# Performance work log

Hardware: AMD Instinct MI355X
Metric: run time of the kernel (lower is better)

Reference implementation:

```python
import jax, jax.numpy as jnp
import numpy as np

B_SZ = 512
D1_IN = 40    # input_dim_first (features)
T = 1024      # input_dim_second (time)
D1_OUT = 120  # output_dim_first
D2_OUT = 64   # output_dim_second


def setup_inputs() -> dict:
    key = jax.random.key(0)
    k_x, k_w1, k_w2, k_b = jax.random.split(key, 4)
    x = jax.random.normal(k_x, (B_SZ, D1_IN, T), dtype=jnp.float32)
    # kaiming-uniform-like init for W1/W2, faithful W init: zeros with 1/T diagonal
    bound1 = 1.0 / np.sqrt(D1_IN)
    W1 = jax.random.uniform(k_w1, (D1_OUT, D1_IN), minval=-bound1, maxval=bound1, dtype=jnp.float32)
    W = jnp.eye(T, dtype=jnp.float32) / T
    bound2 = 1.0 / np.sqrt(T)
    W2 = jax.random.uniform(k_w2, (T, D2_OUT), minval=-bound2, maxval=bound2, dtype=jnp.float32)
    B = jax.random.uniform(k_b, (D1_OUT, D2_OUT), minval=-bound1, maxval=bound1, dtype=jnp.float32)
    lambda_param = jnp.full((1,), 0.5, dtype=jnp.float32)
    return {"x": x, "W1": W1, "W": W, "W2": W2, "B": B, "lambda_param": lambda_param}


def reference(x, W1, W, W2, B, lambda_param):
    # X_bar[b] = W1 @ x[b]  -> [B, D1_OUT, T]
    X_bar = jnp.einsum("of,bft->bot", W1, x)
    # E[b] = x[b] @ W       -> [B, D1_IN, T]; softmax over time axis
    E = jnp.einsum("bft,ts->bfs", x, W)
    A = jax.nn.softmax(E, axis=2)
    lam = jnp.clip(lambda_param, 0.0, 1.0)  # scalar in [1]
    # gather attention rows via modulo indexing: row j uses A[:, j % D1_IN]
    idx = jnp.arange(D1_OUT) % D1_IN
    A_g = A[:, idx, :]                       # [B, D1_OUT, T]
    X_tilde = lam * X_bar * A_g + (1.0 - lam) * X_bar
    out = jnp.einsum("bot,ts->bos", X_tilde, W2) + B[None, :, :]
    out = jax.nn.relu(out)
    return (out, A)
```

## Files before the change

### kernel.cpp

```cpp
#include <hip/hip_runtime.h>
#include <cstdint>
#include <cstddef>

typedef __attribute__((ext_vector_type(8))) short bf16x8;
typedef __attribute__((ext_vector_type(4))) float f32x4;
typedef __attribute__((ext_vector_type(4))) unsigned short ushort4v;
typedef __attribute__((ext_vector_type(2))) unsigned int uint2v;

#define B_SZ   512
#define D1_IN  40
#define T_DIM  1024
#define D1_OUT 120
#define D2_OUT 64
#define OUT0_SZ (B_SZ * D1_OUT * D2_OUT)

__device__ unsigned int g_wmask[8];

__device__ __forceinline__ unsigned short f2bf(float f) {
    unsigned int u = __float_as_uint(f);
    u += 0x7FFFu + ((u >> 16) & 1u);
    return (unsigned short)(u >> 16);
}
__device__ __forceinline__ float bf2f(unsigned int h) {
    return __uint_as_float(h << 16);
}
__device__ __forceinline__ void gld16v(const void* g, void* l) {
    __builtin_amdgcn_global_load_lds(
        (const __attribute__((address_space(1))) unsigned int*)g,
        (__attribute__((address_space(3))) unsigned int*)l, 16, 0, 0);
}

__global__ __launch_bounds__(256) void k_prep_small(const float* __restrict__ W1,
                                                    const float* __restrict__ W,
                                                    const float* __restrict__ W2,
                                                    unsigned short* __restrict__ w2g,
                                                    unsigned short* __restrict__ w1p) {
    int blk = blockIdx.x, tid = threadIdx.x;
    if (blk < 64) {
        __shared__ float tile[32][33];
        int c0 = (blk & 1) * 32, r0 = (blk >> 1) * 32;
        int tx = tid & 31, ty = tid >> 5;
        #pragma unroll
        for (int i = 0; i < 4; i++)
            tile[ty + i * 8][tx] = W2[(size_t)(r0 + ty + i * 8) * D2_OUT + c0 + tx];
        __syncthreads();
        #pragma unroll
        for (int i = 0; i < 4; i++) {
            int s = c0 + ty + i * 8;
            int t = r0 + tx;
            size_t idx = ((size_t)(t >> 6) * 64 + s) * 64
                       + ((((t >> 3) & 7) ^ (s & 7)) << 3) + (t & 7);
            w2g[idx] = f2bf(tile[tx][ty + i * 8]);
        }
    } else if (blk < 72) {
        __shared__ unsigned int sm[256];
        int bn = blk - 64;
        int rbase = tid >> 5, c0 = (tid & 31) * 4;
        unsigned int m = 0;
        for (int ks = 0; ks < 32; ks++) {
            bool nz = false;
            #pragma unroll
            for (int i = 0; i < 4; i++) {
                int r = ks * 32 + rbase + i * 8;
                float4 v = *(const float4*)(W + (size_t)r * T_DIM + bn * 128 + c0);
                nz |= (v.x != 0.f) | (v.y != 0.f) | (v.z != 0.f) | (v.w != 0.f);
            }
            if (nz) m |= (1u << ks);
        }
        sm[tid] = m;
        __syncthreads();
        if (tid == 0) {
            unsigned int acc = 0;
            for (int i = 0; i < 256; i++) acc |= sm[i];
            g_wmask[bn] = acc;
        }
    } else {
        for (int i = tid; i < 128 * 64; i += 256) {
            int o = i >> 6, f = i & 63;
            w1p[i] = (o < D1_OUT && f < D1_IN) ? f2bf(W1[o * D1_IN + f]) : (unsigned short)0;
        }
    }
}

__global__ __launch_bounds__(256) void k_wfrag(const float* __restrict__ W,
                                               unsigned short* __restrict__ wfrag) {
    __shared__ float tl[32 * 132];
    int bn = blockIdx.x >> 5, ks = blockIdx.x & 31;
    int tid = threadIdx.x;
    int k0 = ks * 32, c0 = bn * 128;
    for (int i = tid; i < 1024; i += 256) {
        int r = i >> 5, c4 = i & 31;
        float4 v = *(const float4*)(W + (size_t)(k0 + r) * T_DIM + c0 + c4 * 4);
        *(float4*)&tl[r * 132 + c4 * 4] = v;
    }
    __syncthreads();
    int l = tid & 63, v = tid >> 6;
    int rr = l & 15, q = l >> 4;
    #pragma unroll
    for (int nn = 0; nn < 2; nn++) {
        int n = v + nn * 4;
        bf16x8 o;
        #pragma unroll
        for (int j = 0; j < 8; j++)
            o[j] = (short)f2bf(tl[(q * 8 + j) * 132 + n * 16 + rr]);
        *(bf16x8*)(wfrag + (((size_t)(bn * 32 + ks) * 8 + n) * 512) + (size_t)l * 8) = o;
    }
}

__global__ __launch_bounds__(512) void k_gemm1sm(const float* __restrict__ x,
                                                 const unsigned short* __restrict__ wfrag,
                                                 const float* __restrict__ lamp,
                                                 float* __restrict__ A,
                                                 unsigned short* __restrict__ gab) {
    __shared__ unsigned short xs[16 * 1032];
    __shared__ float red[16][9];
    int row0 = blockIdx.x * 16;
    int tid = threadIdx.x, l = tid & 63, w = tid >> 6;
    int rr = l & 15, q = l >> 4;
    unsigned int mask = g_wmask[w];
    float lam = fminf(fmaxf(lamp[0], 0.f), 1.f), oml = 1.f - lam;
    f32x4 acc[8] = {};

    {
        int r = tid >> 5, c = tid & 31;
        const float* xrow = x + (size_t)(row0 + r) * T_DIM;
        #pragma unroll
        for (int it = 0; it < 8; it++) {
            int c4 = c + it * 32;
            float4 v = *(const float4*)(xrow + c4 * 4);
            ushort4v o;
            o.x = (unsigned short)(__float_as_uint(v.x) >> 16);
            o.y = (unsigned short)(__float_as_uint(v.y) >> 16);
            o.z = (unsigned short)(__float_as_uint(v.z) >> 16);
            o.w = (unsigned short)(__float_as_uint(v.w) >> 16);
            *(ushort4v*)&xs[r * 1032 + c4 * 4] = o;
        }
    }
    __syncthreads();

    for (int ks = 0; ks < 32; ks++) {
        if (!((mask >> ks) & 1u)) continue;
        bf16x8 bx = *(const bf16x8*)&xs[rr * 1032 + ks * 32 + q * 8];
        const unsigned short* wp = wfrag + ((size_t)(w * 32 + ks) * 8) * 512 + (size_t)l * 8;
        #pragma unroll
        for (int n = 0; n < 8; n++) {
            bf16x8 af = *(const bf16x8*)(wp + (size_t)n * 512);
            acc[n] = __builtin_amdgcn_mfma_f32_16x16x32_bf16(af, bx, acc[n], 0, 0, 0);
        }
    }

    float mx = -3.4e38f;
    #pragma unroll
    for (int n = 0; n < 8; n++)
        #pragma unroll
        for (int jj = 0; jj < 4; jj++) mx = fmaxf(mx, acc[n][jj]);
    mx = fmaxf(mx, __shfl_xor(mx, 16));
    mx = fmaxf(mx, __shfl_xor(mx, 32));
    if (l < 16) red[rr][w] = mx;
    __syncthreads();
    float g = red[rr][0];
    #pragma unroll
    for (int ww = 1; ww < 8; ww++) g = fmaxf(g, red[rr][ww]);
    __syncthreads();
    float s = 0.f;
    #pragma unroll
    for (int n = 0; n < 8; n++)
        #pragma unroll
        for (int jj = 0; jj < 4; jj++) {
            float p = __expf(acc[n][jj] - g);
            acc[n][jj] = p;
            s += p;
        }
    s += __shfl_xor(s, 16);
    s += __shfl_xor(s, 32);
    if (l < 16) red[rr][w] = s;
    __syncthreads();
    float tot = 0.f;
    #pragma unroll
    for (int ww = 0; ww < 8; ww++) tot += red[rr][ww];
    float inv = 1.f / tot;
    int rowA = row0 + rr;
    size_t rowg = (size_t)rowA * T_DIM + w * 128;
    int bb = rowA / D1_IN, ff = rowA % D1_IN;
    size_t gbase = (size_t)bb * 16 * 2560 + (size_t)ff * 64;
    #pragma unroll
    for (int n = 0; n < 8; n++) {
        f32x4 o;
        o.x = acc[n][0] * inv; o.y = acc[n][1] * inv;
        o.z = acc[n][2] * inv; o.w = acc[n][3] * inv;
        *(f32x4*)&A[rowg + n * 16 + q * 4] = o;
        int t = w * 128 + n * 16 + q * 4;
        uint2v pk;
        pk.x = (unsigned int)f2bf(lam * o.x + oml) | ((unsigned int)f2bf(lam * o.y + oml) << 16);
        pk.y = (unsigned int)f2bf(lam * o.z + oml) | ((unsigned int)f2bf(lam * o.w + oml) << 16);
        *(uint2v*)&gab[gbase + (size_t)(t >> 6) * 2560 + (t & 63)] = pk;
    }
}

__global__ __launch_bounds__(512) void k_fused(const float* __restrict__ x,
                                               const unsigned short* __restrict__ gab,
                                               const unsigned short* __restrict__ w1p,
                                               const unsigned short* __restrict__ w2g,
                                               const float* __restrict__ Bias,
                                               float* __restrict__ out) {
    __shared__ float xfst[2][10 * 260];
    __shared__ unsigned short gs16[2][5 * 528];
    __shared__ unsigned short w2s[64 * 64];
    __shared__ unsigned short xbt[64 * 72];
    __shared__ unsigned short xtl[128 * 72];
    int b = blockIdx.x;
    int tid = threadIdx.x, l = tid & 63, w = tid >> 6;
    int rr = l & 15, q = l >> 4;
    bf16x8 aw[2];
    #pragma unroll
    for (int ks = 0; ks < 2; ks++)
        aw[ks] = *(const bf16x8*)(w1p + (w * 16 + rr) * 64 + ks * 32 + q * 8);
    int og = w * 16 + rr;
    int am = og % D1_IN;
    int gofs = (am >> 3) * 528 + (am & 7) * 64;
    f32x4 acc2[4] = {};
    const float* xb = x + (size_t)b * D1_IN * T_DIM;
    const unsigned short* gb = gab + (size_t)b * 16 * 2560;

    auto STAGE_XG = [&](int buf, int tc) {
        int t0 = tc * 64;
        int f = w * 4 + (l >> 4);
        gld16v(xb + (size_t)f * T_DIM + t0 + (l & 15) * 4, &xfst[buf][w * 260]);
        if (w < 2) {
            int f2 = 32 + w * 4 + (l >> 4);
            gld16v(xb + (size_t)f2 * T_DIM + t0 + (l & 15) * 4, &xfst[buf][(8 + w) * 260]);
        }
        if (w < 5)
            gld16v(gb + (size_t)tc * 2560 + w * 512 + l * 8, &gs16[buf][w * 528]);
    };
    auto STAGE_W2 = [&](int tc) {
        gld16v(w2g + (size_t)tc * 4096 + w * 512 + l * 8, &w2s[w * 512]);
    };
    auto CONVERT = [&](int buf) {
        if (tid < 320) {
            int g = tid >> 5, tp = tid & 31;
            const float* src = &xfst[buf][g * 260 + 2 * tp];
            float a0 = src[0],   b0 = src[1];
            float a1 = src[64],  b1 = src[65];
            float a2 = src[128], b2 = src[129];
            float a3 = src[192], b3 = src[193];
            uint2v lo, hi;
            lo.x = (unsigned int)f2bf(a0) | ((unsigned int)f2bf(a1) << 16);
            lo.y = (unsigned int)f2bf(a2) | ((unsigned int)f2bf(a3) << 16);
            hi.x = (unsigned int)f2bf(b0) | ((unsigned int)f2bf(b1) << 16);
            hi.y = (unsigned int)f2bf(b2) | ((unsigned int)f2bf(b3) << 16);
            int t = 2 * tp;
            *(uint2v*)&xbt[t * 72 + g * 4] = lo;
            *(uint2v*)&xbt[(t + 1) * 72 + g * 4] = hi;
        }
    };

    {
        int t = tid >> 3, k = tid & 7;
        *(uint2v*)&xbt[t * 72 + 40 + k * 4] = (uint2v){0u, 0u};
    }
    STAGE_XG(0, 0);
    __syncthreads();
    for (int tc = 0; tc < 16; tc++) {
        int cur = tc & 1;
        CONVERT(cur);
        STAGE_W2(tc);
        __syncthreads();
        if (tc < 15) STAGE_XG(cur ^ 1, tc + 1);
        f32x4 acc1[4] = {};
        #pragma unroll
        for (int ni = 0; ni < 4; ni++)
            #pragma unroll
            for (int ks = 0; ks < 2; ks++) {
                bf16x8 bx = *(const bf16x8*)&xbt[(ni * 16 + rr) * 72 + ks * 32 + q * 8];
                acc1[ni] = __builtin_amdgcn_mfma_f32_16x16x32_bf16(bx, aw[ks], acc1[ni], 0, 0, 0);
            }
        const unsigned short* gr = &gs16[cur][gofs];
        #pragma unroll
        for (int ni = 0; ni < 4; ni++) {
            uint2 gp = *(const uint2*)(gr + ni * 16 + q * 4);
            float e0 = acc1[ni][0] * bf2f(gp.x & 0xFFFFu);
            float e1 = acc1[ni][1] * bf2f(gp.x >> 16);
            float e2 = acc1[ni][2] * bf2f(gp.y & 0xFFFFu);
            float e3 = acc1[ni][3] * bf2f(gp.y >> 16);
            uint2 pk;
            pk.x = (unsigned int)f2bf(e0) | ((unsigned int)f2bf(e1) << 16);
            pk.y = (unsigned int)f2bf(e2) | ((unsigned int)f2bf(e3) << 16);
            *(uint2*)&xtl[og * 72 + ni * 16 + q * 4] = pk;
        }
        #pragma unroll
        for (int ks2 = 0; ks2 < 2; ks2++) {
            bf16x8 a2 = *(const bf16x8*)&xtl[og * 72 + ks2 * 32 + q * 8];
            #pragma unroll
            for (int ni = 0; ni < 4; ni++) {
                int s = ni * 16 + rr;
                bf16x8 b2 = *(const bf16x8*)&w2s[s * 64 + (((ks2 * 4 + q) ^ (s & 7)) << 3)];
                acc2[ni] = __builtin_amdgcn_mfma_f32_16x16x32_bf16(a2, b2, acc2[ni], 0, 0, 0);
            }
        }
        __syncthreads();
    }
    #pragma unroll
    for (int ni = 0; ni < 4; ni++)
        #pragma unroll
        for (int j = 0; j < 4; j++) {
            int row = w * 16 + q * 4 + j;
            if (row < D1_OUT) {
                int col = ni * 16 + rr;
                float v = acc2[ni][j] + Bias[row * D2_OUT + col];
                out[((size_t)b * D1_OUT + row) * D2_OUT + col] = fmaxf(v, 0.f);
            }
        }
}

extern "C" void kernel_launch(void* const* d_in, const int* in_sizes, int n_in,
                              void* d_out, int out_size, void* d_ws, size_t ws_size,
                              hipStream_t stream) {
    const float* x    = (const float*)d_in[0];
    const float* W1   = (const float*)d_in[1];
    const float* W    = (const float*)d_in[2];
    const float* W2   = (const float*)d_in[3];
    const float* Bias = (const float*)d_in[4];
    const float* lam  = (const float*)d_in[5];
    float* out = (float*)d_out;
    float* A   = out + OUT0_SZ;

    char* ws = (char*)d_ws;
    unsigned short* gab   = (unsigned short*)(ws);
    unsigned short* wfrag = (unsigned short*)(ws + 41943040);
    unsigned short* w2g   = (unsigned short*)(ws + 44040192);
    unsigned short* w1p   = (unsigned short*)(ws + 44171264);

    hipLaunchKernelGGL(k_prep_small, dim3(73), dim3(256), 0, stream, W1, W, W2, w2g, w1p);
    hipLaunchKernelGGL(k_wfrag, dim3(256), dim3(256), 0, stream, W, wfrag);
    hipLaunchKernelGGL(k_gemm1sm, dim3(1280), dim3(512), 0, stream, x, wfrag, lam, A, gab);
    hipLaunchKernelGGL(k_fused, dim3(512), dim3(512), 0, stream, x, gab, w1p, w2g, Bias, out);
}
```

Baseline: 114.8 us.

## Drop bf16 gate buffer; read fp32 A in fused kernel, persistent softmax kernel

The softmax kernel no longer writes a separate bf16 gating tensor (lam*A+1-lam). The fused kernel now streams the fp32 A output directly and applies the lambda blend in registers. This removes a 40MB-class intermediate write and its layout transform, at the cost of reading A in fp32, twice the bytes of the old gate read. The softmax kernel also becomes persistent with 512 blocks and double-buffers the x tile, prefetching the next rows into registers while it computes.

```diff
diff --git a/kernel.cpp b/kernel.cpp
--- a/kernel.cpp
+++ b/kernel.cpp
@@ -20,9 +20,6 @@
     unsigned int u = __float_as_uint(f);
     u += 0x7FFFu + ((u >> 16) & 1u);
     return (unsigned short)(u >> 16);
-}
-__device__ __forceinline__ float bf2f(unsigned int h) {
-    return __uint_as_float(h << 16);
 }
 __device__ __forceinline__ void gld16v(const void* g, void* l) {
     __builtin_amdgcn_global_load_lds(
@@ -109,129 +106,129 @@
 
 __global__ __launch_bounds__(512) void k_gemm1sm(const float* __restrict__ x,
                                                  const unsigned short* __restrict__ wfrag,
-                                                 const float* __restrict__ lamp,
-                                                 float* __restrict__ A,
-                                                 unsigned short* __restrict__ gab) {
-    __shared__ unsigned short xs[16 * 1032];
-    __shared__ float red[16][9];
-    int row0 = blockIdx.x * 16;
+                                                 float* __restrict__ A) {
+    __shared__ unsigned short xs[2][16 * 1032];
+    __shared__ float red[2][16][9];
     int tid = threadIdx.x, l = tid & 63, w = tid >> 6;
     int rr = l & 15, q = l >> 4;
+    int r = tid >> 5, c = tid & 31;
     unsigned int mask = g_wmask[w];
-    float lam = fminf(fmaxf(lamp[0], 0.f), 1.f), oml = 1.f - lam;
-    f32x4 acc[8] = {};
-
+
+    f32x4 xv[8];
     {
-        int r = tid >> 5, c = tid & 31;
-        const float* xrow = x + (size_t)(row0 + r) * T_DIM;
+        const float* xrow = x + (size_t)(blockIdx.x * 16 + r) * T_DIM;
+        #pragma unroll
+        for (int it = 0; it < 8; it++)
+            xv[it] = *(const f32x4*)(xrow + (c + it * 32) * 4);
+    }
+    int buf = 0;
+    for (int p = blockIdx.x; p < 1280; p += 512, buf ^= 1) {
         #pragma unroll
         for (int it = 0; it < 8; it++) {
-            int c4 = c + it * 32;
-            float4 v = *(const float4*)(xrow + c4 * 4);
             ushort4v o;
-            o.x = (unsigned short)(__float_as_uint(v.x) >> 16);
-            o.y = (unsigned short)(__float_as_uint(v.y) >> 16);
-            o.z = (unsigned short)(__float_as_uint(v.z) >> 16);
-            o.w = (unsigned short)(__float_as_uint(v.w) >> 16);
-            *(ushort4v*)&xs[r * 1032 + c4 * 4] = o;
-        }
-    }
-    __syncthreads();
-
-    for (int ks = 0; ks < 32; ks++) {
-        if (!((mask >> ks) & 1u)) continue;
-        bf16x8 bx = *(const bf16x8*)&xs[rr * 1032 + ks * 32 + q * 8];
-        const unsigned short* wp = wfrag + ((size_t)(w * 32 + ks) * 8) * 512 + (size_t)l * 8;
+            o.x = (unsigned short)(__float_as_uint(xv[it].x) >> 16);
+            o.y = (unsigned short)(__float_as_uint(xv[it].y) >> 16);
+            o.z = (unsigned short)(__float_as_uint(xv[it].z) >> 16);
+            o.w = (unsigned short)(__float_as_uint(xv[it].w) >> 16);
+            *(ushort4v*)&xs[buf][r * 1032 + (c + it * 32) * 4] = o;
+        }
+        __syncthreads();
+        int pn = p + 512;
+        if (pn < 1280) {
+            const float* xrow = x + (size_t)(pn * 16 + r) * T_DIM;
+            #pragma unroll
+            for (int it = 0; it < 8; it++)
+                xv[it] = *(const f32x4*)(xrow + (c + it * 32) * 4);
+        }
+        f32x4 acc[8] = {};
+        for (int ks = 0; ks < 32; ks++) {
+            if (!((mask >> ks) & 1u)) continue;
+            bf16x8 bx = *(const bf16x8*)&xs[buf][rr * 1032 + ks * 32 + q * 8];
+            const unsigned short* wp = wfrag + ((size_t)(w * 32 + ks) * 8) * 512 + (size_t)l * 8;
+            #pragma unroll
+            for (int n = 0; n < 8; n++) {
+                bf16x8 af = *(const bf16x8*)(wp + (size_t)n * 512);
+                acc[n] = __builtin_amdgcn_mfma_f32_16x16x32_bf16(af, bx, acc[n], 0, 0, 0);
+            }
+        }
+        float mx = -3.4e38f;
+        #pragma unroll
+        for (int n = 0; n < 8; n++)
+            #pragma unroll
+            for (int jj = 0; jj < 4; jj++) mx = fmaxf(mx, acc[n][jj]);
+        mx = fmaxf(mx, __shfl_xor(mx, 16));
+        mx = fmaxf(mx, __shfl_xor(mx, 32));
+        if (l < 16) red[buf][rr][w] = mx;
+        __syncthreads();
+        float g = red[buf][rr][0];
+        #pragma unroll
+        for (int ww = 1; ww < 8; ww++) g = fmaxf(g, red[buf][rr][ww]);
+        __syncthreads();
+        float s = 0.f;
+        #pragma unroll
+        for (int n = 0; n < 8; n++)
+            #pragma unroll
+            for (int jj = 0; jj < 4; jj++) {
+                float pp = __expf(acc[n][jj] - g);
+                acc[n][jj] = pp;
+                s += pp;
+            }
+        s += __shfl_xor(s, 16);
+        s += __shfl_xor(s, 32);
+        if (l < 16) red[buf][rr][w] = s;
+        __syncthreads();
+        float tot = 0.f;
+        #pragma unroll
+        for (int ww = 0; ww < 8; ww++) tot += red[buf][rr][ww];
+        float inv = 1.f / tot;
+        size_t rowg = (size_t)(p * 16 + rr) * T_DIM + w * 128;
         #pragma unroll
         for (int n = 0; n < 8; n++) {
-            bf16x8 af = *(const bf16x8*)(wp + (size_t)n * 512);
-            acc[n] = __builtin_amdgcn_mfma_f32_16x16x32_bf16(af, bx, acc[n], 0, 0, 0);
-        }
-    }
-
-    float mx = -3.4e38f;
-    #pragma unroll
-    for (int n = 0; n < 8; n++)
-        #pragma unroll
-        for (int jj = 0; jj < 4; jj++) mx = fmaxf(mx, acc[n][jj]);
-    mx = fmaxf(mx, __shfl_xor(mx, 16));
-    mx = fmaxf(mx, __shfl_xor(mx, 32));
-    if (l < 16) red[rr][w] = mx;
-    __syncthreads();
-    float g = red[rr][0];
-    #pragma unroll
-    for (int ww = 1; ww < 8; ww++) g = fmaxf(g, red[rr][ww]);
-    __syncthreads();
-    float s = 0.f;
-    #pragma unroll
-    for (int n = 0; n < 8; n++)
-        #pragma unroll
-        for (int jj = 0; jj < 4; jj++) {
-            float p = __expf(acc[n][jj] - g);
-            acc[n][jj] = p;
-            s += p;
-        }
-    s += __shfl_xor(s, 16);
-    s += __shfl_xor(s, 32);
-    if (l < 16) red[rr][w] = s;
-    __syncthreads();
-    float tot = 0.f;
-    #pragma unroll
-    for (int ww = 0; ww < 8; ww++) tot += red[rr][ww];
-    float inv = 1.f / tot;
-    int rowA = row0 + rr;
-    size_t rowg = (size_t)rowA * T_DIM + w * 128;
-    int bb = rowA / D1_IN, ff = rowA % D1_IN;
-    size_t gbase = (size_t)bb * 16 * 2560 + (size_t)ff * 64;
-    #pragma unroll
-    for (int n = 0; n < 8; n++) {
-        f32x4 o;
-        o.x = acc[n][0] * inv; o.y = acc[n][1] * inv;
-        o.z = acc[n][2] * inv; o.w = acc[n][3] * inv;
-        *(f32x4*)&A[rowg + n * 16 + q * 4] = o;
-        int t = w * 128 + n * 16 + q * 4;
-        uint2v pk;
-        pk.x = (unsigned int)f2bf(lam * o.x + oml) | ((unsigned int)f2bf(lam * o.y + oml) << 16);
-        pk.y = (unsigned int)f2bf(lam * o.z + oml) | ((unsigned int)f2bf(lam * o.w + oml) << 16);
-        *(uint2v*)&gab[gbase + (size_t)(t >> 6) * 2560 + (t & 63)] = pk;
+            f32x4 o;
+            o.x = acc[n][0] * inv; o.y = acc[n][1] * inv;
+            o.z = acc[n][2] * inv; o.w = acc[n][3] * inv;
+            *(f32x4*)&A[rowg + n * 16 + q * 4] = o;
+        }
     }
 }
 
 __global__ __launch_bounds__(512) void k_fused(const float* __restrict__ x,
-                                               const unsigned short* __restrict__ gab,
+                                               const float* __restrict__ A,
                                                const unsigned short* __restrict__ w1p,
                                                const unsigned short* __restrict__ w2g,
                                                const float* __restrict__ Bias,
+                                               const float* __restrict__ lamp,
                                                float* __restrict__ out) {
     __shared__ float xfst[2][10 * 260];
-    __shared__ unsigned short gs16[2][5 * 528];
+    __shared__ float gst[2][10 * 260];
     __shared__ unsigned short w2s[64 * 64];
     __shared__ unsigned short xbt[64 * 72];
     __shared__ unsigned short xtl[128 * 72];
     int b = blockIdx.x;
     int tid = threadIdx.x, l = tid & 63, w = tid >> 6;
     int rr = l & 15, q = l >> 4;
+    float lam = fminf(fmaxf(lamp[0], 0.f), 1.f), oml = 1.f - lam;
     bf16x8 aw[2];
     #pragma unroll
     for (int ks = 0; ks < 2; ks++)
         aw[ks] = *(const bf16x8*)(w1p + (w * 16 + rr) * 64 + ks * 32 + q * 8);
     int og = w * 16 + rr;
     int am = og % D1_IN;
-    int gofs = (am >> 3) * 528 + (am & 7) * 64;
+    int amg = (am >> 2) * 260 + (am & 3) * 64;
     f32x4 acc2[4] = {};
     const float* xb = x + (size_t)b * D1_IN * T_DIM;
-    const unsigned short* gb = gab + (size_t)b * 16 * 2560;
+    const float* Ab = A + (size_t)b * D1_IN * T_DIM;
 
     auto STAGE_XG = [&](int buf, int tc) {
         int t0 = tc * 64;
         int f = w * 4 + (l >> 4);
         gld16v(xb + (size_t)f * T_DIM + t0 + (l & 15) * 4, &xfst[buf][w * 260]);
+        gld16v(Ab + (size_t)f * T_DIM + t0 + (l & 15) * 4, &gst[buf][w * 260]);
         if (w < 2) {
             int f2 = 32 + w * 4 + (l >> 4);
             gld16v(xb + (size_t)f2 * T_DIM + t0 + (l & 15) * 4, &xfst[buf][(8 + w) * 260]);
-        }
-        if (w < 5)
-            gld16v(gb + (size_t)tc * 2560 + w * 512 + l * 8, &gs16[buf][w * 528]);
+            gld16v(Ab + (size_t)f2 * T_DIM + t0 + (l & 15) * 4, &gst[buf][(8 + w) * 260]);
+        }
     };
     auto STAGE_W2 = [&](int tc) {
         gld16v(w2g + (size_t)tc * 4096 + w * 512 + l * 8, &w2s[w * 512]);
@@ -275,14 +272,14 @@
                 bf16x8 bx = *(const bf16x8*)&xbt[(ni * 16 + rr) * 72 + ks * 32 + q * 8];
                 acc1[ni] = __builtin_amdgcn_mfma_f32_16x16x32_bf16(bx, aw[ks], acc1[ni], 0, 0, 0);
             }
-        const unsigned short* gr = &gs16[cur][gofs];
+        const float* gr = &gst[cur][amg];
         #pragma unroll
         for (int ni = 0; ni < 4; ni++) {
-            uint2 gp = *(const uint2*)(gr + ni * 16 + q * 4);
-            float e0 = acc1[ni][0] * bf2f(gp.x & 0xFFFFu);
-            float e1 = acc1[ni][1] * bf2f(gp.x >> 16);
-            float e2 = acc1[ni][2] * bf2f(gp.y & 0xFFFFu);
-            float e3 = acc1[ni][3] * bf2f(gp.y >> 16);
+            f32x4 gv = *(const f32x4*)(gr + ni * 16 + q * 4);
+            float e0 = acc1[ni][0] * (lam * gv.x + oml);
+            float e1 = acc1[ni][1] * (lam * gv.y + oml);
+            float e2 = acc1[ni][2] * (lam * gv.z + oml);
+            float e3 = acc1[ni][3] * (lam * gv.w + oml);
             uint2 pk;
             pk.x = (unsigned int)f2bf(e0) | ((unsigned int)f2bf(e1) << 16);
             pk.y = (unsigned int)f2bf(e2) | ((unsigned int)f2bf(e3) << 16);
@@ -326,13 +323,12 @@
     float* A   = out + OUT0_SZ;
 
     char* ws = (char*)d_ws;
-    unsigned short* gab   = (unsigned short*)(ws);
-    unsigned short* wfrag = (unsigned short*)(ws + 41943040);
-    unsigned short* w2g   = (unsigned short*)(ws + 44040192);
-    unsigned short* w1p   = (unsigned short*)(ws + 44171264);
+    unsigned short* wfrag = (unsigned short*)(ws);
+    unsigned short* w2g   = (unsigned short*)(ws + 2097152);
+    unsigned short* w1p   = (unsigned short*)(ws + 2228224);
 
     hipLaunchKernelGGL(k_prep_small, dim3(73), dim3(256), 0, stream, W1, W, W2, w2g, w1p);
     hipLaunchKernelGGL(k_wfrag, dim3(256), dim3(256), 0, stream, W, wfrag);
-    hipLaunchKernelGGL(k_gemm1sm, dim3(1280), dim3(512), 0, stream, x, wfrag, lam, A, gab);
-    hipLaunchKernelGGL(k_fused, dim3(512), dim3(512), 0, stream, x, gab, w1p, w2g, Bias, out);
-}
+    hipLaunchKernelGGL(k_gemm1sm, dim3(512), dim3(512), 0, stream, x, wfrag, A);
+    hipLaunchKernelGGL(k_fused, dim3(512), dim3(512), 0, stream, x, A, w1p, w2g, Bias, lam, out);
+}
```

Measured after the change: 245.9 us. 2.14x slower.

## Fuse softmax attention GEMM into per-batch fused kernel

Applied to the files above, without the earlier changes.

Merges the attention GEMM+softmax kernel into the main fused kernel so each block first computes the 40 softmax rows of its batch, writes A and the gating buffer, then runs the projection stage. This removes one kernel launch and lets the gating data be reread while it is likely still in cache. The cost is that x fragments are now read directly from global memory instead of through shared memory. Work per block also grows and grid parallelism drops from 1280 blocks to 512 for the first phase. The last 16-row tile wastes half its MFMA work on clamped padding rows.

```diff
diff --git a/kernel.cpp b/kernel.cpp
--- a/kernel.cpp
+++ b/kernel.cpp
@@ -107,110 +107,180 @@
     }
 }
 
-__global__ __launch_bounds__(512) void k_gemm1sm(const float* __restrict__ x,
-                                                 const unsigned short* __restrict__ wfrag,
-                                                 const float* __restrict__ lamp,
-                                                 float* __restrict__ A,
-                                                 unsigned short* __restrict__ gab) {
-    __shared__ unsigned short xs[16 * 1032];
-    __shared__ float red[16][9];
-    int row0 = blockIdx.x * 16;
-    int tid = threadIdx.x, l = tid & 63, w = tid >> 6;
-    int rr = l & 15, q = l >> 4;
-    unsigned int mask = g_wmask[w];
-    float lam = fminf(fmaxf(lamp[0], 0.f), 1.f), oml = 1.f - lam;
-    f32x4 acc[8] = {};
-
-    {
-        int r = tid >> 5, c = tid & 31;
-        const float* xrow = x + (size_t)(row0 + r) * T_DIM;
-        #pragma unroll
-        for (int it = 0; it < 8; it++) {
-            int c4 = c + it * 32;
-            float4 v = *(const float4*)(xrow + c4 * 4);
-            ushort4v o;
-            o.x = (unsigned short)(__float_as_uint(v.x) >> 16);
-            o.y = (unsigned short)(__float_as_uint(v.y) >> 16);
-            o.z = (unsigned short)(__float_as_uint(v.z) >> 16);
-            o.w = (unsigned short)(__float_as_uint(v.w) >> 16);
-            *(ushort4v*)&xs[r * 1032 + c4 * 4] = o;
-        }
-    }
-    __syncthreads();
-
-    for (int ks = 0; ks < 32; ks++) {
-        if (!((mask >> ks) & 1u)) continue;
-        bf16x8 bx = *(const bf16x8*)&xs[rr * 1032 + ks * 32 + q * 8];
-        const unsigned short* wp = wfrag + ((size_t)(w * 32 + ks) * 8) * 512 + (size_t)l * 8;
-        #pragma unroll
-        for (int n = 0; n < 8; n++) {
-            bf16x8 af = *(const bf16x8*)(wp + (size_t)n * 512);
-            acc[n] = __builtin_amdgcn_mfma_f32_16x16x32_bf16(af, bx, acc[n], 0, 0, 0);
-        }
-    }
-
-    float mx = -3.4e38f;
-    #pragma unroll
-    for (int n = 0; n < 8; n++)
-        #pragma unroll
-        for (int jj = 0; jj < 4; jj++) mx = fmaxf(mx, acc[n][jj]);
-    mx = fmaxf(mx, __shfl_xor(mx, 16));
-    mx = fmaxf(mx, __shfl_xor(mx, 32));
-    if (l < 16) red[rr][w] = mx;
-    __syncthreads();
-    float g = red[rr][0];
-    #pragma unroll
-    for (int ww = 1; ww < 8; ww++) g = fmaxf(g, red[rr][ww]);
-    __syncthreads();
-    float s = 0.f;
-    #pragma unroll
-    for (int n = 0; n < 8; n++)
-        #pragma unroll
-        for (int jj = 0; jj < 4; jj++) {
-            float p = __expf(acc[n][jj] - g);
-            acc[n][jj] = p;
-            s += p;
-        }
-    s += __shfl_xor(s, 16);
-    s += __shfl_xor(s, 32);
-    if (l < 16) red[rr][w] = s;
-    __syncthreads();
-    float tot = 0.f;
-    #pragma unroll
-    for (int ww = 0; ww < 8; ww++) tot += red[rr][ww];
-    float inv = 1.f / tot;
-    int rowA = row0 + rr;
-    size_t rowg = (size_t)rowA * T_DIM + w * 128;
-    int bb = rowA / D1_IN, ff = rowA % D1_IN;
-    size_t gbase = (size_t)bb * 16 * 2560 + (size_t)ff * 64;
-    #pragma unroll
-    for (int n = 0; n < 8; n++) {
-        f32x4 o;
-        o.x = acc[n][0] * inv; o.y = acc[n][1] * inv;
-        o.z = acc[n][2] * inv; o.w = acc[n][3] * inv;
-        *(f32x4*)&A[rowg + n * 16 + q * 4] = o;
-        int t = w * 128 + n * 16 + q * 4;
-        uint2v pk;
-        pk.x = (unsigned int)f2bf(lam * o.x + oml) | ((unsigned int)f2bf(lam * o.y + oml) << 16);
-        pk.y = (unsigned int)f2bf(lam * o.z + oml) | ((unsigned int)f2bf(lam * o.w + oml) << 16);
-        *(uint2v*)&gab[gbase + (size_t)(t >> 6) * 2560 + (t & 63)] = pk;
-    }
-}
-
-__global__ __launch_bounds__(512) void k_fused(const float* __restrict__ x,
-                                               const unsigned short* __restrict__ gab,
-                                               const unsigned short* __restrict__ w1p,
-                                               const unsigned short* __restrict__ w2g,
-                                               const float* __restrict__ Bias,
-                                               float* __restrict__ out) {
+__global__ __launch_bounds__(512) void k_mega(const float* __restrict__ x,
+                                              const unsigned short* __restrict__ wfrag,
+                                              const unsigned short* __restrict__ w1p,
+                                              const unsigned short* __restrict__ w2g,
+                                              const float* __restrict__ Bias,
+                                              const float* __restrict__ lamp,
+                                              float* __restrict__ A,
+                                              unsigned short* __restrict__ gbuf,
+                                              float* __restrict__ out) {
     __shared__ float xfst[2][10 * 260];
     __shared__ unsigned short gs16[2][5 * 528];
     __shared__ unsigned short w2s[64 * 64];
     __shared__ unsigned short xbt[64 * 72];
     __shared__ unsigned short xtl[128 * 72];
+    __shared__ float red[32][9];
     int b = blockIdx.x;
     int tid = threadIdx.x, l = tid & 63, w = tid >> 6;
     int rr = l & 15, q = l >> 4;
+    float lam = fminf(fmaxf(lamp[0], 0.f), 1.f), oml = 1.f - lam;
+    unsigned int mask = g_wmask[w];
+    unsigned short* gb = gbuf + (size_t)b * 16 * 2560;
+
+    auto MKFRAG = [&](const float* xrow, int off, bf16x8& o) {
+        f32x4 a0 = *(const f32x4*)(xrow + off);
+        f32x4 b0 = *(const f32x4*)(xrow + off + 4);
+        ((unsigned int*)&o)[0] = (__float_as_uint(a0.x) >> 16) | (__float_as_uint(a0.y) & 0xFFFF0000u);
+        ((unsigned int*)&o)[1] = (__float_as_uint(a0.z) >> 16) | (__float_as_uint(a0.w) & 0xFFFF0000u);
+        ((unsigned int*)&o)[2] = (__float_as_uint(b0.x) >> 16) | (__float_as_uint(b0.y) & 0xFFFF0000u);
+        ((unsigned int*)&o)[3] = (__float_as_uint(b0.z) >> 16) | (__float_as_uint(b0.w) & 0xFFFF0000u);
+    };
+    auto SOFTMAX_STORE = [&](f32x4* acc, int m, bool valid) {
+        float mx = -3.4e38f;
+        #pragma unroll
+        for (int n = 0; n < 8; n++)
+            #pragma unroll
+            for (int jj = 0; jj < 4; jj++) mx = fmaxf(mx, acc[n][jj]);
+        mx = fmaxf(mx, __shfl_xor(mx, 16));
+        mx = fmaxf(mx, __shfl_xor(mx, 32));
+        if (l < 16) red[m * 16 + rr][w] = mx;
+    };
+
+    {
+        const float* xrow0 = x + (size_t)(b * 40 + rr) * T_DIM;
+        const float* xrow1 = x + (size_t)(b * 40 + 16 + rr) * T_DIM;
+        f32x4 acc[2][8] = {};
+        for (int ks = 0; ks < 32; ks++) {
+            if (!((mask >> ks) & 1u)) continue;
+            int off = ks * 32 + q * 8;
+            bf16x8 bx0, bx1;
+            MKFRAG(xrow0, off, bx0);
+            MKFRAG(xrow1, off, bx1);
+            const unsigned short* wp = wfrag + ((size_t)(w * 32 + ks) * 8) * 512 + (size_t)l * 8;
+            #pragma unroll
+            for (int n = 0; n < 8; n++) {
+                bf16x8 af = *(const bf16x8*)(wp + (size_t)n * 512);
+                acc[0][n] = __builtin_amdgcn_mfma_f32_16x16x32_bf16(af, bx0, acc[0][n], 0, 0, 0);
+                acc[1][n] = __builtin_amdgcn_mfma_f32_16x16x32_bf16(af, bx1, acc[1][n], 0, 0, 0);
+            }
+        }
+        #pragma unroll
+        for (int m = 0; m < 2; m++) SOFTMAX_STORE(acc[m], m, true);
+        __syncthreads();
+        float gm[2];
+        #pragma unroll
+        for (int m = 0; m < 2; m++) {
+            float g = red[m * 16 + rr][0];
+            #pragma unroll
+            for (int ww = 1; ww < 8; ww++) g = fmaxf(g, red[m * 16 + rr][ww]);
+            gm[m] = g;
+        }
+        __syncthreads();
+        #pragma unroll
+        for (int m = 0; m < 2; m++) {
+            float s = 0.f;
+            #pragma unroll
+            for (int n = 0; n < 8; n++)
+                #pragma unroll
+                for (int jj = 0; jj < 4; jj++) {
+                    float p = __expf(acc[m][n][jj] - gm[m]);
+                    acc[m][n][jj] = p;
+                    s += p;
+                }
+            s += __shfl_xor(s, 16);
+            s += __shfl_xor(s, 32);
+            if (l < 16) red[m * 16 + rr][w] = s;
+        }
+        __syncthreads();
+        #pragma unroll
+        for (int m = 0; m < 2; m++) {
+            float tot = 0.f;
+            #pragma unroll
+            for (int ww = 0; ww < 8; ww++) tot += red[m * 16 + rr][ww];
+            float inv = 1.f / tot;
+            int f = m * 16 + rr;
+            size_t rowg = (size_t)(b * 40 + f) * T_DIM + w * 128;
+            #pragma unroll
+            for (int n = 0; n < 8; n++) {
+                f32x4 o;
+                o.x = acc[m][n][0] * inv; o.y = acc[m][n][1] * inv;
+                o.z = acc[m][n][2] * inv; o.w = acc[m][n][3] * inv;
+                *(f32x4*)&A[rowg + n * 16 + q * 4] = o;
+                uint2v pk;
+                pk.x = (unsigned int)f2bf(lam * o.x + oml) | ((unsigned int)f2bf(lam * o.y + oml) << 16);
+                pk.y = (unsigned int)f2bf(lam * o.z + oml) | ((unsigned int)f2bf(lam * o.w + oml) << 16);
+                *(uint2v*)&gb[(size_t)(w * 2 + (n >> 2)) * 2560 + f * 64 + (n & 3) * 16 + q * 4] = pk;
+            }
+        }
+        __syncthreads();
+    }
+    {
+        int rowa = b * 40 + 32 + rr;
+        int rowc = rowa < 20480 ? rowa : 20479;
+        const float* xrowB = x + (size_t)rowc * T_DIM;
+        f32x4 acc[8] = {};
+        for (int ks = 0; ks < 32; ks++) {
+            if (!((mask >> ks) & 1u)) continue;
+            int off = ks * 32 + q * 8;
+            bf16x8 bxB;
+            MKFRAG(xrowB, off, bxB);
+            const unsigned short* wp = wfrag + ((size_t)(w * 32 + ks) * 8) * 512 + (size_t)l * 8;
+            #pragma unroll
+            for (int n = 0; n < 8; n++) {
+                bf16x8 af = *(const bf16x8*)(wp + (size_t)n * 512);
+                acc[n] = __builtin_amdgcn_mfma_f32_16x16x32_bf16(af, bxB, acc[n], 0, 0, 0);
+            }
+        }
+        float mx = -3.4e38f;
+        #pragma unroll
+        for (int n = 0; n < 8; n++)
+            #pragma unroll
+            for (int jj = 0; jj < 4; jj++) mx = fmaxf(mx, acc[n][jj]);
+        mx = fmaxf(mx, __shfl_xor(mx, 16));
+        mx = fmaxf(mx, __shfl_xor(mx, 32));
+        if (l < 16) red[rr][w] = mx;
+        __syncthreads();
+        float g = red[rr][0];
+        #pragma unroll
+        for (int ww = 1; ww < 8; ww++) g = fmaxf(g, red[rr][ww]);
+        __syncthreads();
+        float s = 0.f;
+        #pragma unroll
+        for (int n = 0; n < 8; n++)
+            #pragma unroll
+            for (int jj = 0; jj < 4; jj++) {
+                float p = __expf(acc[n][jj] - g);
+                acc[n][jj] = p;
+                s += p;
+            }
+        s += __shfl_xor(s, 16);
+        s += __shfl_xor(s, 32);
+        if (l < 16) red[rr][w] = s;
+        __syncthreads();
+        if (rr < 8) {
+            float tot = 0.f;
+            #pragma unroll
+            for (int ww = 0; ww < 8; ww++) tot += red[rr][ww];
+            float inv = 1.f / tot;
+            int f = 32 + rr;
+            size_t rowg = (size_t)(b * 40 + f) * T_DIM + w * 128;
+            #pragma unroll
+            for (int n = 0; n < 8; n++) {
+                f32x4 o;
+                o.x = acc[n][0] * inv; o.y = acc[n][1] * inv;
+                o.z = acc[n][2] * inv; o.w = acc[n][3] * inv;
+                *(f32x4*)&A[rowg + n * 16 + q * 4] = o;
+                uint2v pk;
+                pk.x = (unsigned int)f2bf(lam * o.x + oml) | ((unsigned int)f2bf(lam * o.y + oml) << 16);
+                pk.y = (unsigned int)f2bf(lam * o.z + oml) | ((unsigned int)f2bf(lam * o.w + oml) << 16);
+                *(uint2v*)&gb[(size_t)(w * 2 + (n >> 2)) * 2560 + f * 64 + (n & 3) * 16 + q * 4] = pk;
+            }
+        }
+    }
+    __syncthreads();
+
     bf16x8 aw[2];
     #pragma unroll
     for (int ks = 0; ks < 2; ks++)
@@ -220,7 +290,6 @@
     int gofs = (am >> 3) * 528 + (am & 7) * 64;
     f32x4 acc2[4] = {};
     const float* xb = x + (size_t)b * D1_IN * T_DIM;
-    const unsigned short* gb = gab + (size_t)b * 16 * 2560;
 
     auto STAGE_XG = [&](int buf, int tc) {
         int t0 = tc * 64;
@@ -326,13 +395,12 @@
     float* A   = out + OUT0_SZ;
 
     char* ws = (char*)d_ws;
-    unsigned short* gab   = (unsigned short*)(ws);
+    unsigned short* gbuf  = (unsigned short*)(ws);
     unsigned short* wfrag = (unsigned short*)(ws + 41943040);
     unsigned short* w2g   = (unsigned short*)(ws + 44040192);
     unsigned short* w1p   = (unsigned short*)(ws + 44171264);
 
     hipLaunchKernelGGL(k_prep_small, dim3(73), dim3(256), 0, stream, W1, W, W2, w2g, w1p);
     hipLaunchKernelGGL(k_wfrag, dim3(256), dim3(256), 0, stream, W, wfrag);
-    hipLaunchKernelGGL(k_gemm1sm, dim3(1280), dim3(512), 0, stream, x, wfrag, lam, A, gab);
-    hipLaunchKernelGGL(k_fused, dim3(512), dim3(512), 0, stream, x, gab, w1p, w2g, Bias, out);
-}
+    hipLaunchKernelGGL(k_mega, dim3(512), dim3(512), 0, stream, x, wfrag, w1p, w2g, Bias, lam, A, gbuf, out);
+}
```

Measured after the change: 101.1 us. 1.13x faster.
